# Performance work log

Measured on AMD Instinct MI355X. Metric: run time of the kernel, lower is better.

## Reference

```python
import jax, jax.numpy as jnp
import numpy as np

B, C, H, W = 8, 512, 32, 32
NH, DH = 8, 64          # num_heads, head_dim (C = NH*DH)
GROUPS, EPS = 32, 1e-5


def group_norm(x, gamma, beta):
    b, c, h, w = x.shape
    xg = x.reshape(b, GROUPS, c // GROUPS, h, w)
    mu = xg.mean(axis=(2, 3, 4), keepdims=True)
    var = xg.var(axis=(2, 3, 4), keepdims=True)
    xn = ((xg - mu) * jax.lax.rsqrt(var + EPS)).reshape(b, c, h, w)
    return xn * gamma[:, None, None] + beta[:, None, None]


def conv1x1(x, w, b):
    # x: [B,C,H,W], w: [O,C], b: [O]
    return jnp.einsum('bchw,oc->bohw', x, w) + b[:, None, None]


def setup_inputs() -> dict:
    key = jax.random.key(0)
    ks = jax.random.split(key, 5)
    return {
        'x': jax.random.normal(ks[0], (B, C, H, W), jnp.float32),
        'norm_gamma': jnp.ones((C,), jnp.float32),
        'norm_beta': jnp.zeros((C,), jnp.float32),
        'qkv_w': jax.random.normal(ks[1], (3 * C, C), jnp.float32) * (1.0 / np.sqrt(C)),
        'qkv_b': jax.random.normal(ks[2], (3 * C,), jnp.float32) * 0.02,
        'proj_w': jax.random.normal(ks[3], (C, C), jnp.float32) * (1.0 / np.sqrt(C)),
        'proj_b': jax.random.normal(ks[4], (C,), jnp.float32) * 0.02,
    }


def reference(x, norm_gamma, norm_beta, qkv_w, qkv_b, proj_w, proj_b):
    scale = DH ** -0.5
    h = group_norm(x, norm_gamma, norm_beta)
    qkv = conv1x1(h, qkv_w, qkv_b)                       # [B,3C,H,W]
    qkv = qkv.reshape(B, 3, NH, DH, H * W)
    qkv = jnp.transpose(qkv, (1, 0, 2, 4, 3))            # [3,B,NH,HW,DH]
    q, k, v = qkv[0], qkv[1], qkv[2]
    attn = jnp.einsum('bhid,bhjd->bhij', q, k) * scale   # [B,NH,HW,HW]
    attn = jax.nn.softmax(attn, axis=-1)
    h = jnp.einsum('bhij,bhjd->bhid', attn, v)           # [B,NH,HW,DH]
    # faithful to torch: direct row-major reshape [B,NH,HW,DH] -> [B,C,H,W]
    h = h.reshape(B, C, H, W)
    h = conv1x1(h, proj_w, proj_b)
    return x + h
```

## Files before the change

kernel.cpp:

```cpp
#include <hip/hip_runtime.h>


typedef float  f32x4  __attribute__((ext_vector_type(4)));
typedef float  f32x16 __attribute__((ext_vector_type(16)));
typedef __bf16 bf16x8 __attribute__((ext_vector_type(8)));
typedef __bf16 bf16x4 __attribute__((ext_vector_type(4)));
typedef __bf16 bf16x2 __attribute__((ext_vector_type(2)));

#define MFMA(a, b, c)   __builtin_amdgcn_mfma_f32_16x16x32_bf16(a, b, c, 0, 0, 0)
#define MFMA32(a, b, c) __builtin_amdgcn_mfma_f32_32x32x16_bf16(a, b, c, 0, 0, 0)

__device__ __forceinline__ void async16(const __bf16* g, __bf16* l) {
  __builtin_amdgcn_global_load_lds((const __attribute__((address_space(1))) void*)g,
                                   (__attribute__((address_space(3))) void*)l, 16, 0, 0);
}

__device__ __forceinline__ int chk(int n, int c) {
  return ((((n >> 6) * 16 + (c >> 5)) * 4 + ((c >> 3) & 3)) * 512) + (n & 63) * 8 + (c & 7);
}

__global__ __launch_bounds__(512) void prep_k(const float* __restrict__ x,
                                              const float* __restrict__ gamma,
                                              const float* __restrict__ beta,
                                              __bf16* __restrict__ Hout,
                                              const float* __restrict__ qw, __bf16* __restrict__ dq,
                                              const float* __restrict__ pw, __bf16* __restrict__ dp) {
  __shared__ __bf16 xs[16 * 1032];
  __shared__ float  red[16];
  __shared__ float  ga[16], be[16], stat[2];
  const int tid = threadIdx.x;

  if (blockIdx.x >= 256) {
    int i = ((blockIdx.x - 256) * 512 + tid) * 4;
    const float* src = (i < 786432) ? qw : pw;
    __bf16* dst = (i < 786432) ? dq : dp;
    int j = (i < 786432) ? i : (i - 786432);
    int m = j >> 9, k = j & 511;
    float4 v = *(const float4*)(src + j);
    bf16x4 o;
    o[0] = (__bf16)v.x; o[1] = (__bf16)v.y; o[2] = (__bf16)v.z; o[3] = (__bf16)v.w;
    *(bf16x4*)(dst + chk(m, k)) = o;
    return;
  }

  const int w = tid >> 6, l = tid & 63;
  const int bg = blockIdx.x, b = bg >> 5, g = bg & 31, c0 = g * 16;
  const float* xg = x + b * 524288 + c0 * 1024;

  float sum = 0.f, sq = 0.f;
#pragma unroll
  for (int p = 0; p < 8; p++) {
    int idx = p * 2048 + tid * 4;
    float4 v = *(const float4*)(xg + idx);
    int c = idx >> 10, s = idx & 1023;
    bf16x4 o;
    o[0] = (__bf16)v.x; o[1] = (__bf16)v.y; o[2] = (__bf16)v.z; o[3] = (__bf16)v.w;
    *(bf16x4*)(&xs[c * 1032 + s]) = o;
    sum += v.x + v.y + v.z + v.w;
    sq  += v.x * v.x + v.y * v.y + v.z * v.z + v.w * v.w;
  }
#pragma unroll
  for (int o = 32; o > 0; o >>= 1) { sum += __shfl_down(sum, o); sq += __shfl_down(sq, o); }
  if (l == 0) { red[w * 2] = sum; red[w * 2 + 1] = sq; }
  __syncthreads();
  if (tid == 0) {
    float S = 0.f, Q = 0.f;
#pragma unroll
    for (int i = 0; i < 8; i++) { S += red[i * 2]; Q += red[i * 2 + 1]; }
    float mean = S * (1.f / 16384.f);
    float var  = Q * (1.f / 16384.f) - mean * mean;
    stat[0] = mean; stat[1] = rsqrtf(var + 1e-5f);
  }
  if (tid < 16) { ga[tid] = gamma[c0 + tid]; be[tid] = beta[c0 + tid]; }
  __syncthreads();
  const float mean = stat[0], rstd = stat[1];
#pragma unroll
  for (int p = 0; p < 2; p++) {
    int s = p * 512 + tid;
    int n = b * 1024 + s;
    bf16x8 o0, o1;
#pragma unroll
    for (int c = 0; c < 8; c++) {
      float f = (float)xs[c * 1032 + s];
      o0[c] = (__bf16)((f - mean) * rstd * ga[c] + be[c]);
    }
#pragma unroll
    for (int c = 8; c < 16; c++) {
      float f = (float)xs[c * 1032 + s];
      o1[c - 8] = (__bf16)((f - mean) * rstd * ga[c] + be[c]);
    }
    *(bf16x8*)(Hout + chk(n, c0)) = o0;
    *(bf16x8*)(Hout + chk(n, c0 + 8)) = o1;
  }
}

__global__ __launch_bounds__(256) void gemm_qkv_k(const __bf16* __restrict__ W,
                                                  const float* __restrict__ bias,
                                                  const __bf16* __restrict__ H,
                                                  __bf16* __restrict__ qbuf,
                                                  __bf16* __restrict__ kbuf,
                                                  __bf16* __restrict__ vt) {
  __shared__ union {
    struct { __bf16 a[2][4096]; __bf16 b[2][4096]; } ab;
    __bf16 cs[128 * 136];
  } lds;
  const int tid = threadIdx.x;
  const int w = tid >> 6, l = tid & 63, quad = l >> 4, li = l & 15;
  const int wr = w >> 1, wc = w & 1;
  const int mblk = blockIdx.x >> 6, nblk = blockIdx.x & 63;
  const int m0 = mblk * 128, n0 = nblk * 128;

  f32x4 acc[4][4];
#pragma unroll
  for (int i = 0; i < 4; i++)
#pragma unroll
    for (int j = 0; j < 4; j++) acc[i][j] = f32x4{0.f, 0.f, 0.f, 0.f};

  const __bf16* Ag = W + (((m0 >> 6) * 16) * 4 + w) * 512 + l * 8;
  const __bf16* Bg = H + (((n0 >> 6) * 16) * 4 + w) * 512 + l * 8;
  const int halfA = 16 * 4 * 512;

  async16(Ag,         &lds.ab.a[0][w * 1024]);
  async16(Ag + halfA, &lds.ab.a[0][w * 1024 + 512]);
  async16(Bg,         &lds.ab.b[0][w * 1024]);
  async16(Bg + halfA, &lds.ab.b[0][w * 1024 + 512]);

#pragma unroll 1
  for (int kt = 0; kt < 16; kt++) {
    int cur = kt & 1, nxt = cur ^ 1;
    __syncthreads();
    if (kt < 15) {
      int ko = (kt + 1) * 2048;
      async16(Ag + ko,          &lds.ab.a[nxt][w * 1024]);
      async16(Ag + halfA + ko,  &lds.ab.a[nxt][w * 1024 + 512]);
      async16(Bg + ko,          &lds.ab.b[nxt][w * 1024]);
      async16(Bg + halfA + ko,  &lds.ab.b[nxt][w * 1024 + 512]);
    }
    bf16x8 af[4], bfr[4];
#pragma unroll
    for (int i = 0; i < 4; i++)
      af[i] = *(const bf16x8*)(&lds.ab.a[cur][quad * 1024 + (wr * 64 + i * 16 + li) * 8]);
#pragma unroll
    for (int i = 0; i < 4; i++)
      bfr[i] = *(const bf16x8*)(&lds.ab.b[cur][quad * 1024 + (wc * 64 + i * 16 + li) * 8]);
#pragma unroll
    for (int i = 0; i < 4; i++)
#pragma unroll
      for (int j = 0; j < 4; j++) acc[i][j] = MFMA(af[i], bfr[j], acc[i][j]);
  }

  const int t = m0 >> 9;
  const int cbase = m0 & 511;
  __syncthreads();
#pragma unroll
  for (int mi = 0; mi < 4; mi++) {
    int olocal = wr * 64 + mi * 16 + quad * 4;
    float bs[4];
#pragma unroll
    for (int r = 0; r < 4; r++) bs[r] = bias[m0 + olocal + r];
#pragma unroll
    for (int ni = 0; ni < 4; ni++) {
      int nlocal = wc * 64 + ni * 16 + li;
      bf16x4 pk;
#pragma unroll
      for (int r = 0; r < 4; r++) {
        float f = acc[mi][ni][r] + bs[r];
        if (t == 0) f *= 0.180336880f;
        pk[r] = (__bf16)f;
      }
      *(bf16x4*)(&lds.cs[nlocal * 136 + olocal]) = pk;
    }
  }
  __syncthreads();
  const int bb = n0 >> 10, s0 = n0 & 1023;
  if (t < 2) {
    __bf16* dst = (t == 0) ? qbuf : kbuf;
    const int nh0 = cbase >> 6;
#pragma unroll
    for (int p = 0; p < 8; p++) {
      int idx = p * 256 + tid;
      int oc = idx & 15, nloc = idx >> 4;
      uint4 val = *(const uint4*)(&lds.cs[nloc * 136 + oc * 8]);
      int bh = bb * 8 + nh0 + (oc >> 3);
      int s = s0 + nloc, d0 = (oc & 7) * 8;
      *(uint4*)(dst + (((bh * 16 + (s >> 6)) * 8 + (d0 >> 3)) * 64 + (s & 63)) * 8) = val;
    }
  } else {
#pragma unroll
    for (int p = 0; p < 8; p++) {
      int idx = p * 256 + tid;
      int o = idx & 127, ng = idx >> 7;
      int c = cbase + o, nh2 = c >> 6, d = c & 63;
      int bh = bb * 8 + nh2;
      int j0 = s0 + ng * 8;
      bf16x8 vv;
#pragma unroll
      for (int jj = 0; jj < 8; jj++) vv[jj] = lds.cs[(ng * 8 + jj) * 136 + o];
      *(bf16x8*)(vt + (((bh * 16 + (j0 >> 6)) * 8 + ((j0 >> 3) & 7)) * 64 + d) * 8) = vv;
    }
  }
}

__global__ __launch_bounds__(256) void attn_k(const __bf16* __restrict__ qb,
                                              const __bf16* __restrict__ kb,
                                              const __bf16* __restrict__ vt,
                                              __bf16* __restrict__ pin) {
  __shared__ __bf16 KC[2][4096];
  __shared__ __bf16 VC[2][4096];
  __shared__ __bf16 PO[8192];
  const int tid = threadIdx.x;
  const int w = tid >> 6, l = tid & 63, hi = l >> 5, i32 = l & 31;
  const int x = blockIdx.x;
  const int qt = (x >> 3) & 7;
  const int bh = (x & 7) | ((x >> 6) << 3);
  const int b = bh >> 3, nh = bh & 7;
  const __bf16* Qg = qb + bh * 65536;
  const __bf16* Kg = kb + bh * 65536;
  const __bf16* Vg = vt + bh * 65536;

#pragma unroll
  for (int p = 0; p < 2; p++) {
    int ch = w + 4 * p;
    async16(Kg + ch * 512 + l * 8, &KC[0][ch * 512 + l * 8]);
    async16(Vg + ch * 512 + l * 8, &VC[0][ch * 512 + l * 8]);
  }

  const int s = qt * 128 + w * 32 + i32;
  bf16x8 qf[4];
#pragma unroll
  for (int ks = 0; ks < 4; ks++)
    qf[ks] = *(const bf16x8*)(Qg + ((s >> 6) * 8 + ks * 2 + hi) * 512 + (s & 63) * 8);

  __syncthreads();

  const int swz = (i32 & 7) << 4;
  char* Pw = (char*)PO + w * 4096;
  float lsum = 0.f;
  f32x16 oacc[2];
#pragma unroll
  for (int r = 0; r < 16; r++) { oacc[0][r] = 0.f; oacc[1][r] = 0.f; }

#pragma unroll 1
  for (int kv = 0; kv < 16; kv++) {
    int cur = kv & 1, nxt = cur ^ 1;
    if (kv < 15) {
#pragma unroll
      for (int p = 0; p < 2; p++) {
        int ch = w + 4 * p;
        async16(Kg + (kv + 1) * 4096 + ch * 512 + l * 8, &KC[nxt][ch * 512 + l * 8]);
        async16(Vg + (kv + 1) * 4096 + ch * 512 + l * 8, &VC[nxt][ch * 512 + l * 8]);
      }
    }

    f32x16 st[2];
#pragma unroll
    for (int r = 0; r < 16; r++) { st[0][r] = 0.f; st[1][r] = 0.f; }
#pragma unroll
    for (int ks = 0; ks < 4; ks++) {
#pragma unroll
      for (int jt = 0; jt < 2; jt++) {
        bf16x8 kf = *(const bf16x8*)(&KC[cur][(ks * 2 + hi) * 512 + (jt * 32 + i32) * 8]);
        st[jt] = MFMA32(kf, qf[ks], st[jt]);
      }
    }

#pragma unroll
    for (int jt = 0; jt < 2; jt++) {
#pragma unroll
      for (int q2 = 0; q2 < 4; q2++) {
        float p0 = __builtin_amdgcn_exp2f(st[jt][q2 * 4 + 0]);
        float p1 = __builtin_amdgcn_exp2f(st[jt][q2 * 4 + 1]);
        float p2 = __builtin_amdgcn_exp2f(st[jt][q2 * 4 + 2]);
        float p3 = __builtin_amdgcn_exp2f(st[jt][q2 * 4 + 3]);
        lsum += (p0 + p1) + (p2 + p3);
        bf16x4 pk;
        pk[0] = (__bf16)p0; pk[1] = (__bf16)p1; pk[2] = (__bf16)p2; pk[3] = (__bf16)p3;
        *(bf16x4*)(Pw + ((i32 * 128 + jt * 64 + q2 * 16 + hi * 8) ^ swz)) = pk;
      }
    }

#pragma unroll
    for (int js = 0; js < 4; js++) {
      bf16x8 pf = *(const bf16x8*)(Pw + ((i32 * 128 + js * 32 + hi * 16) ^ swz));
#pragma unroll
      for (int dt = 0; dt < 2; dt++) {
        bf16x8 vf = *(const bf16x8*)(&VC[cur][(js * 2 + hi) * 512 + (dt * 32 + i32) * 8]);
        oacc[dt] = MFMA32(pf, vf, oacc[dt]);
      }
    }
    __syncthreads();
  }

  lsum += __shfl_xor(lsum, 32);
  const float inv = 1.f / lsum;

#pragma unroll
  for (int dt = 0; dt < 2; dt++) {
#pragma unroll
    for (int r = 0; r < 8; r++) {
      int ilo = (r & 3) + 8 * (r >> 2) + 4 * hi;
      float iblo = __shfl(inv, ilo);
      float ibhi = __shfl(inv, ilo + 16);
      bf16x2 ov;
      ov[0] = (__bf16)(oacc[dt][r]     * iblo);
      ov[1] = (__bf16)(oacc[dt][r + 8] * ibhi);
      *(bf16x2*)((char*)PO + (ilo * 64 + dt * 32 + i32) * 16 + w * 4) = ov;
    }
  }
  __syncthreads();
  __bf16* Pg = pin + (nh * 8 + qt) * 65536 + b * 8192;
#pragma unroll
  for (int p = 0; p < 4; p++) {
    int idx = p * 256 + tid;
    *(bf16x8*)(Pg + idx * 8) = *(const bf16x8*)((const char*)PO + idx * 16);
  }
}

__global__ __launch_bounds__(256) void gemm_proj_k(const __bf16* __restrict__ W,
                                                   const float* __restrict__ bias,
                                                   const __bf16* __restrict__ P,
                                                   const float* __restrict__ x,
                                                   float* __restrict__ out) {
  __shared__ __bf16 AL[2][2048];
  __shared__ __bf16 BL[2][4096];
  const int tid = threadIdx.x;
  const int w = tid >> 6, l = tid & 63, quad = l >> 4, li = l & 15;
  const int wr = w >> 1, wc = w & 1;
  const int mblk = blockIdx.x >> 6, nblk = blockIdx.x & 63;
  const int m0 = mblk * 64, n0 = nblk * 128;

  f32x4 acc[2][4];
#pragma unroll
  for (int i = 0; i < 2; i++)
#pragma unroll
    for (int j = 0; j < 4; j++) acc[i][j] = f32x4{0.f, 0.f, 0.f, 0.f};

  const __bf16* Ag = W + ((mblk * 16) * 4 + w) * 512 + l * 8;
  const __bf16* Bg = P + w * 65536 + (n0 + l) * 8;

  async16(Ag,       &AL[0][w * 512]);
  async16(Bg,       &BL[0][w * 1024]);
  async16(Bg + 512, &BL[0][w * 1024 + 512]);

#pragma unroll 1
  for (int kt = 0; kt < 16; kt++) {
    int cur = kt & 1, nxt = cur ^ 1;
    __syncthreads();
    if (kt < 15) {
      int koA = (kt + 1) * 2048;
      int koB = (kt + 1) * 262144;
      async16(Ag + koA,       &AL[nxt][w * 512]);
      async16(Bg + koB,       &BL[nxt][w * 1024]);
      async16(Bg + koB + 512, &BL[nxt][w * 1024 + 512]);
    }
    bf16x8 af[2], bfr[4];
#pragma unroll
    for (int i = 0; i < 2; i++)
      af[i] = *(const bf16x8*)(&AL[cur][quad * 512 + (wr * 32 + i * 16 + li) * 8]);
#pragma unroll
    for (int j = 0; j < 4; j++)
      bfr[j] = *(const bf16x8*)(&BL[cur][quad * 1024 + (wc * 64 + j * 16 + li) * 8]);
#pragma unroll
    for (int i = 0; i < 2; i++)
#pragma unroll
      for (int j = 0; j < 4; j++) acc[i][j] = MFMA(af[i], bfr[j], acc[i][j]);
  }

  const int bb = n0 >> 10;
#pragma unroll
  for (int mi = 0; mi < 2; mi++) {
    int o = m0 + wr * 32 + mi * 16 + quad * 4;
    float bs[4];
#pragma unroll
    for (int r = 0; r < 4; r++) bs[r] = bias[o + r];
#pragma unroll
    for (int ni = 0; ni < 4; ni++) {
      int n = n0 + wc * 64 + ni * 16 + li;
      int s = n & 1023;
#pragma unroll
      for (int r = 0; r < 4; r++) {
        int a = (bb * 512 + o + r) * 1024 + s;
        out[a] = acc[mi][ni][r] + bs[r] + x[a];
      }
    }
  }
}

extern "C" void kernel_launch(void* const* d_in, const int* in_sizes, int n_in,
                              void* d_out, int out_size, void* d_ws, size_t ws_size,
                              hipStream_t stream) {
  const float* x      = (const float*)d_in[0];
  const float* gamma  = (const float*)d_in[1];
  const float* beta   = (const float*)d_in[2];
  const float* qkv_w  = (const float*)d_in[3];
  const float* qkv_b  = (const float*)d_in[4];
  const float* proj_w = (const float*)d_in[5];
  const float* proj_b = (const float*)d_in[6];

  __bf16* ws   = (__bf16*)d_ws;
  __bf16* H    = ws;
  __bf16* qbuf = ws + 4194304;
  __bf16* kbuf = ws + 8388608;
  __bf16* vt   = ws + 12582912;
  __bf16* wq   = ws + 16777216;
  __bf16* wp   = ws + 17563648;

  prep_k<<<768, 512, 0, stream>>>(x, gamma, beta, H, qkv_w, wq, proj_w, wp);
  gemm_qkv_k<<<768, 256, 0, stream>>>(wq, qkv_b, H, qbuf, kbuf, vt);
  attn_k<<<512, 256, 0, stream>>>(qbuf, kbuf, vt, H);
  gemm_proj_k<<<512, 256, 0, stream>>>(wp, proj_b, H, x, (float*)d_out);
}
```

Measured before the change: 143.2 us.

## Fuse all four stages into one persistent kernel with grid barriers

Replaces the four separate launches (groupnorm/weight-convert, QKV GEMM, attention, projection GEMM) with a single 768-block megakernel. The stages are separated by atomic-counter grid barriers, and each stage reuses one shared LDS buffer. The goal is to remove the launch gaps and tail effects between kernels. It relies on all 768 blocks being co-resident (3 per CU under launch bounds), adds spin-barrier and memset overhead, and leaves blocks idle in the 512-block stages. The attention score loop is also reordered so each 32-column tile is computed and exponentiated before the next, which lowers register pressure.

```diff
diff --git a/kernel.cpp b/kernel.cpp
--- a/kernel.cpp
+++ b/kernel.cpp
@@ -19,368 +19,355 @@
   return ((((n >> 6) * 16 + (c >> 5)) * 4 + ((c >> 3) & 3)) * 512) + (n & 63) * 8 + (c & 7);
 }
 
-__global__ __launch_bounds__(512) void prep_k(const float* __restrict__ x,
-                                              const float* __restrict__ gamma,
-                                              const float* __restrict__ beta,
-                                              __bf16* __restrict__ Hout,
-                                              const float* __restrict__ qw, __bf16* __restrict__ dq,
-                                              const float* __restrict__ pw, __bf16* __restrict__ dp) {
-  __shared__ __bf16 xs[16 * 1032];
-  __shared__ float  red[16];
-  __shared__ float  ga[16], be[16], stat[2];
-  const int tid = threadIdx.x;
-
-  if (blockIdx.x >= 256) {
-    int i = ((blockIdx.x - 256) * 512 + tid) * 4;
-    const float* src = (i < 786432) ? qw : pw;
-    __bf16* dst = (i < 786432) ? dq : dp;
-    int j = (i < 786432) ? i : (i - 786432);
-    int m = j >> 9, k = j & 511;
-    float4 v = *(const float4*)(src + j);
-    bf16x4 o;
-    o[0] = (__bf16)v.x; o[1] = (__bf16)v.y; o[2] = (__bf16)v.z; o[3] = (__bf16)v.w;
-    *(bf16x4*)(dst + chk(m, k)) = o;
-    return;
-  }
-
-  const int w = tid >> 6, l = tid & 63;
-  const int bg = blockIdx.x, b = bg >> 5, g = bg & 31, c0 = g * 16;
-  const float* xg = x + b * 524288 + c0 * 1024;
-
-  float sum = 0.f, sq = 0.f;
-#pragma unroll
-  for (int p = 0; p < 8; p++) {
-    int idx = p * 2048 + tid * 4;
-    float4 v = *(const float4*)(xg + idx);
-    int c = idx >> 10, s = idx & 1023;
-    bf16x4 o;
-    o[0] = (__bf16)v.x; o[1] = (__bf16)v.y; o[2] = (__bf16)v.z; o[3] = (__bf16)v.w;
-    *(bf16x4*)(&xs[c * 1032 + s]) = o;
-    sum += v.x + v.y + v.z + v.w;
-    sq  += v.x * v.x + v.y * v.y + v.z * v.z + v.w * v.w;
-  }
-#pragma unroll
-  for (int o = 32; o > 0; o >>= 1) { sum += __shfl_down(sum, o); sq += __shfl_down(sq, o); }
-  if (l == 0) { red[w * 2] = sum; red[w * 2 + 1] = sq; }
+__device__ __forceinline__ void gbar(unsigned* c) {
   __syncthreads();
-  if (tid == 0) {
-    float S = 0.f, Q = 0.f;
-#pragma unroll
-    for (int i = 0; i < 8; i++) { S += red[i * 2]; Q += red[i * 2 + 1]; }
-    float mean = S * (1.f / 16384.f);
-    float var  = Q * (1.f / 16384.f) - mean * mean;
-    stat[0] = mean; stat[1] = rsqrtf(var + 1e-5f);
-  }
-  if (tid < 16) { ga[tid] = gamma[c0 + tid]; be[tid] = beta[c0 + tid]; }
-  __syncthreads();
-  const float mean = stat[0], rstd = stat[1];
-#pragma unroll
-  for (int p = 0; p < 2; p++) {
-    int s = p * 512 + tid;
-    int n = b * 1024 + s;
-    bf16x8 o0, o1;
-#pragma unroll
-    for (int c = 0; c < 8; c++) {
-      float f = (float)xs[c * 1032 + s];
-      o0[c] = (__bf16)((f - mean) * rstd * ga[c] + be[c]);
-    }
-#pragma unroll
-    for (int c = 8; c < 16; c++) {
-      float f = (float)xs[c * 1032 + s];
-      o1[c - 8] = (__bf16)((f - mean) * rstd * ga[c] + be[c]);
-    }
-    *(bf16x8*)(Hout + chk(n, c0)) = o0;
-    *(bf16x8*)(Hout + chk(n, c0 + 8)) = o1;
-  }
-}
-
-__global__ __launch_bounds__(256) void gemm_qkv_k(const __bf16* __restrict__ W,
-                                                  const float* __restrict__ bias,
-                                                  const __bf16* __restrict__ H,
-                                                  __bf16* __restrict__ qbuf,
-                                                  __bf16* __restrict__ kbuf,
-                                                  __bf16* __restrict__ vt) {
-  __shared__ union {
-    struct { __bf16 a[2][4096]; __bf16 b[2][4096]; } ab;
-    __bf16 cs[128 * 136];
-  } lds;
-  const int tid = threadIdx.x;
-  const int w = tid >> 6, l = tid & 63, quad = l >> 4, li = l & 15;
-  const int wr = w >> 1, wc = w & 1;
-  const int mblk = blockIdx.x >> 6, nblk = blockIdx.x & 63;
-  const int m0 = mblk * 128, n0 = nblk * 128;
-
-  f32x4 acc[4][4];
-#pragma unroll
-  for (int i = 0; i < 4; i++)
-#pragma unroll
-    for (int j = 0; j < 4; j++) acc[i][j] = f32x4{0.f, 0.f, 0.f, 0.f};
-
-  const __bf16* Ag = W + (((m0 >> 6) * 16) * 4 + w) * 512 + l * 8;
-  const __bf16* Bg = H + (((n0 >> 6) * 16) * 4 + w) * 512 + l * 8;
-  const int halfA = 16 * 4 * 512;
-
-  async16(Ag,         &lds.ab.a[0][w * 1024]);
-  async16(Ag + halfA, &lds.ab.a[0][w * 1024 + 512]);
-  async16(Bg,         &lds.ab.b[0][w * 1024]);
-  async16(Bg + halfA, &lds.ab.b[0][w * 1024 + 512]);
-
-#pragma unroll 1
-  for (int kt = 0; kt < 16; kt++) {
-    int cur = kt & 1, nxt = cur ^ 1;
-    __syncthreads();
-    if (kt < 15) {
-      int ko = (kt + 1) * 2048;
-      async16(Ag + ko,          &lds.ab.a[nxt][w * 1024]);
-      async16(Ag + halfA + ko,  &lds.ab.a[nxt][w * 1024 + 512]);
-      async16(Bg + ko,          &lds.ab.b[nxt][w * 1024]);
-      async16(Bg + halfA + ko,  &lds.ab.b[nxt][w * 1024 + 512]);
-    }
-    bf16x8 af[4], bfr[4];
-#pragma unroll
-    for (int i = 0; i < 4; i++)
-      af[i] = *(const bf16x8*)(&lds.ab.a[cur][quad * 1024 + (wr * 64 + i * 16 + li) * 8]);
-#pragma unroll
-    for (int i = 0; i < 4; i++)
-      bfr[i] = *(const bf16x8*)(&lds.ab.b[cur][quad * 1024 + (wc * 64 + i * 16 + li) * 8]);
-#pragma unroll
-    for (int i = 0; i < 4; i++)
-#pragma unroll
-      for (int j = 0; j < 4; j++) acc[i][j] = MFMA(af[i], bfr[j], acc[i][j]);
-  }
-
-  const int t = m0 >> 9;
-  const int cbase = m0 & 511;
-  __syncthreads();
-#pragma unroll
-  for (int mi = 0; mi < 4; mi++) {
-    int olocal = wr * 64 + mi * 16 + quad * 4;
-    float bs[4];
-#pragma unroll
-    for (int r = 0; r < 4; r++) bs[r] = bias[m0 + olocal + r];
-#pragma unroll
-    for (int ni = 0; ni < 4; ni++) {
-      int nlocal = wc * 64 + ni * 16 + li;
-      bf16x4 pk;
-#pragma unroll
-      for (int r = 0; r < 4; r++) {
-        float f = acc[mi][ni][r] + bs[r];
-        if (t == 0) f *= 0.180336880f;
-        pk[r] = (__bf16)f;
-      }
-      *(bf16x4*)(&lds.cs[nlocal * 136 + olocal]) = pk;
-    }
+  if (threadIdx.x == 0) {
+    __threadfence();
+    atomicAdd(c, 1u);
+    while (atomicAdd(c, 0u) < 768u) __builtin_amdgcn_s_sleep(8);
+    __threadfence();
   }
   __syncthreads();
-  const int bb = n0 >> 10, s0 = n0 & 1023;
-  if (t < 2) {
-    __bf16* dst = (t == 0) ? qbuf : kbuf;
-    const int nh0 = cbase >> 6;
-#pragma unroll
-    for (int p = 0; p < 8; p++) {
+}
+
+__global__ __launch_bounds__(256, 3) void mega_k(
+    const float* __restrict__ x, const float* __restrict__ gamma, const float* __restrict__ beta,
+    const float* __restrict__ qw, const float* __restrict__ qkv_b,
+    const float* __restrict__ pw, const float* __restrict__ proj_b,
+    __bf16* __restrict__ H, __bf16* __restrict__ qbuf, __bf16* __restrict__ kbuf,
+    __bf16* __restrict__ vt, __bf16* __restrict__ wq, __bf16* __restrict__ wp,
+    float* __restrict__ out, unsigned* __restrict__ bar) {
+  __shared__ __align__(16) char smem[49152];
+  const int tid = threadIdx.x, bid = blockIdx.x;
+
+  if (bid < 256) {
+    __bf16* xs  = (__bf16*)smem;
+    float* red  = (float*)(smem + 33024);
+    float* ga   = (float*)(smem + 33024 + 32);
+    float* be   = ga + 16;
+    float* stat = be + 16;
+    const int w = tid >> 6, l = tid & 63;
+    const int b = bid >> 5, g = bid & 31, c0 = g * 16;
+    const float* xg = x + b * 524288 + c0 * 1024;
+    float sum = 0.f, sq = 0.f;
+#pragma unroll
+    for (int c = 0; c < 16; c++) {
+      float4 v = *(const float4*)(xg + c * 1024 + tid * 4);
+      bf16x4 o;
+      o[0] = (__bf16)v.x; o[1] = (__bf16)v.y; o[2] = (__bf16)v.z; o[3] = (__bf16)v.w;
+      *(bf16x4*)(&xs[c * 1032 + tid * 4]) = o;
+      sum += v.x + v.y + v.z + v.w;
+      sq  += v.x * v.x + v.y * v.y + v.z * v.z + v.w * v.w;
+    }
+#pragma unroll
+    for (int o = 32; o > 0; o >>= 1) { sum += __shfl_down(sum, o); sq += __shfl_down(sq, o); }
+    if (l == 0) { red[w * 2] = sum; red[w * 2 + 1] = sq; }
+    __syncthreads();
+    if (tid == 0) {
+      float S = 0.f, Q = 0.f;
+#pragma unroll
+      for (int i = 0; i < 4; i++) { S += red[i * 2]; Q += red[i * 2 + 1]; }
+      float mean = S * (1.f / 16384.f);
+      float var  = Q * (1.f / 16384.f) - mean * mean;
+      stat[0] = mean; stat[1] = rsqrtf(var + 1e-5f);
+    }
+    if (tid < 16) { ga[tid] = gamma[c0 + tid]; be[tid] = beta[c0 + tid]; }
+    __syncthreads();
+    const float mean = stat[0], rstd = stat[1];
+#pragma unroll
+    for (int p = 0; p < 4; p++) {
+      int sx = p * 256 + tid;
+      int n = b * 1024 + sx;
+      bf16x8 o0, o1;
+#pragma unroll
+      for (int c = 0; c < 8; c++)
+        o0[c] = (__bf16)(((float)xs[c * 1032 + sx] - mean) * rstd * ga[c] + be[c]);
+#pragma unroll
+      for (int c = 8; c < 16; c++)
+        o1[c - 8] = (__bf16)(((float)xs[c * 1032 + sx] - mean) * rstd * ga[c] + be[c]);
+      *(bf16x8*)(H + chk(n, c0)) = o0;
+      *(bf16x8*)(H + chk(n, c0 + 8)) = o1;
+    }
+  } else {
+#pragma unroll
+    for (int sweep = 0; sweep < 2; sweep++) {
+      int i = ((bid - 256) * 256 + tid) * 4 + sweep * 524288;
+      const float* src = (i < 786432) ? qw : pw;
+      __bf16* dst = (i < 786432) ? wq : wp;
+      int j = (i < 786432) ? i : (i - 786432);
+      int m = j >> 9, k = j & 511;
+      float4 v = *(const float4*)(src + j);
+      bf16x4 o;
+      o[0] = (__bf16)v.x; o[1] = (__bf16)v.y; o[2] = (__bf16)v.z; o[3] = (__bf16)v.w;
+      *(bf16x4*)(dst + chk(m, k)) = o;
+    }
+  }
+  gbar(bar + 0);
+
+  {
+    __bf16 (*lA)[4096] = (__bf16(*)[4096])smem;
+    __bf16 (*lB)[4096] = (__bf16(*)[4096])(smem + 16384);
+    __bf16* cs         = (__bf16*)smem;
+    const int w = tid >> 6, l = tid & 63, quad = l >> 4, li = l & 15;
+    const int wr = w >> 1, wc = w & 1;
+    const int mblk = bid >> 6, nblk = bid & 63;
+    const int m0 = mblk * 128, n0 = nblk * 128;
+
+    f32x4 acc[4][4];
+#pragma unroll
+    for (int i = 0; i < 4; i++)
+#pragma unroll
+      for (int j = 0; j < 4; j++) acc[i][j] = f32x4{0.f, 0.f, 0.f, 0.f};
+
+    const __bf16* Ag = wq + (((m0 >> 6) * 16) * 4 + w) * 512 + l * 8;
+    const __bf16* Bg = H  + (((n0 >> 6) * 16) * 4 + w) * 512 + l * 8;
+    const int halfA = 16 * 4 * 512;
+
+    async16(Ag,         &lA[0][w * 1024]);
+    async16(Ag + halfA, &lA[0][w * 1024 + 512]);
+    async16(Bg,         &lB[0][w * 1024]);
+    async16(Bg + halfA, &lB[0][w * 1024 + 512]);
+
+#pragma unroll 1
+    for (int kt = 0; kt < 16; kt++) {
+      int cur = kt & 1, nxt = cur ^ 1;
+      __syncthreads();
+      if (kt < 15) {
+        int ko = (kt + 1) * 2048;
+        async16(Ag + ko,         &lA[nxt][w * 1024]);
+        async16(Ag + halfA + ko, &lA[nxt][w * 1024 + 512]);
+        async16(Bg + ko,         &lB[nxt][w * 1024]);
+        async16(Bg + halfA + ko, &lB[nxt][w * 1024 + 512]);
+      }
+      bf16x8 af[4], bfr[4];
+#pragma unroll
+      for (int i = 0; i < 4; i++)
+        af[i] = *(const bf16x8*)(&lA[cur][quad * 1024 + (wr * 64 + i * 16 + li) * 8]);
+#pragma unroll
+      for (int i = 0; i < 4; i++)
+        bfr[i] = *(const bf16x8*)(&lB[cur][quad * 1024 + (wc * 64 + i * 16 + li) * 8]);
+#pragma unroll
+      for (int i = 0; i < 4; i++)
+#pragma unroll
+        for (int j = 0; j < 4; j++) acc[i][j] = MFMA(af[i], bfr[j], acc[i][j]);
+    }
+
+    const int t = m0 >> 9;
+    const int cbase = m0 & 511;
+    __syncthreads();
+#pragma unroll
+    for (int mi = 0; mi < 4; mi++) {
+      int olocal = wr * 64 + mi * 16 + quad * 4;
+      float bs[4];
+#pragma unroll
+      for (int r = 0; r < 4; r++) bs[r] = qkv_b[m0 + olocal + r];
+#pragma unroll
+      for (int ni = 0; ni < 4; ni++) {
+        int nlocal = wc * 64 + ni * 16 + li;
+        bf16x4 pk;
+#pragma unroll
+        for (int r = 0; r < 4; r++) {
+          float f = acc[mi][ni][r] + bs[r];
+          if (t == 0) f *= 0.180336880f;
+          pk[r] = (__bf16)f;
+        }
+        *(bf16x4*)(&cs[nlocal * 136 + olocal]) = pk;
+      }
+    }
+    __syncthreads();
+    const int bb = n0 >> 10, s0 = n0 & 1023;
+    if (t < 2) {
+      __bf16* dst = (t == 0) ? qbuf : kbuf;
+      const int nh0 = cbase >> 6;
+#pragma unroll
+      for (int p = 0; p < 8; p++) {
+        int idx = p * 256 + tid;
+        int oc = idx & 15, nloc = idx >> 4;
+        uint4 val = *(const uint4*)(&cs[nloc * 136 + oc * 8]);
+        int bh = bb * 8 + nh0 + (oc >> 3);
+        int s = s0 + nloc, d0 = (oc & 7) * 8;
+        *(uint4*)(dst + (((bh * 16 + (s >> 6)) * 8 + (d0 >> 3)) * 64 + (s & 63)) * 8) = val;
+      }
+    } else {
+#pragma unroll
+      for (int p = 0; p < 8; p++) {
+        int idx = p * 256 + tid;
+        int o = idx & 127, ng = idx >> 7;
+        int c = cbase + o, nh2 = c >> 6, d = c & 63;
+        int bh = bb * 8 + nh2;
+        int j0 = s0 + ng * 8;
+        bf16x8 vv;
+#pragma unroll
+        for (int jj = 0; jj < 8; jj++) vv[jj] = cs[(ng * 8 + jj) * 136 + o];
+        *(bf16x8*)(vt + (((bh * 16 + (j0 >> 6)) * 8 + ((j0 >> 3) & 7)) * 64 + d) * 8) = vv;
+      }
+    }
+  }
+  gbar(bar + 1);
+
+  if (bid < 512) {
+    __bf16 (*KC)[4096] = (__bf16(*)[4096])smem;
+    __bf16 (*VC)[4096] = (__bf16(*)[4096])(smem + 16384);
+    __bf16* PO         = (__bf16*)(smem + 32768);
+    const int w = tid >> 6, l = tid & 63, hi = l >> 5, i32 = l & 31;
+    const int qt = (bid >> 3) & 7;
+    const int bh = (bid & 7) | ((bid >> 6) << 3);
+    const int b = bh >> 3, nh = bh & 7;
+    const __bf16* Qg = qbuf + bh * 65536;
+    const __bf16* Kg = kbuf + bh * 65536;
+    const __bf16* Vg = vt   + bh * 65536;
+
+#pragma unroll
+    for (int p = 0; p < 2; p++) {
+      int ch = w + 4 * p;
+      async16(Kg + ch * 512 + l * 8, &KC[0][ch * 512 + l * 8]);
+      async16(Vg + ch * 512 + l * 8, &VC[0][ch * 512 + l * 8]);
+    }
+    const int s = qt * 128 + w * 32 + i32;
+    bf16x8 qf[4];
+#pragma unroll
+    for (int ks = 0; ks < 4; ks++)
+      qf[ks] = *(const bf16x8*)(Qg + ((s >> 6) * 8 + ks * 2 + hi) * 512 + (s & 63) * 8);
+    __syncthreads();
+
+    const int swz = (i32 & 7) << 4;
+    char* Pw = (char*)PO + w * 4096;
+    float lsum = 0.f;
+    f32x16 oacc[2];
+#pragma unroll
+    for (int r = 0; r < 16; r++) { oacc[0][r] = 0.f; oacc[1][r] = 0.f; }
+
+#pragma unroll 1
+    for (int kv = 0; kv < 16; kv++) {
+      int cur = kv & 1, nxt = cur ^ 1;
+      if (kv < 15) {
+#pragma unroll
+        for (int p = 0; p < 2; p++) {
+          int ch = w + 4 * p;
+          async16(Kg + (kv + 1) * 4096 + ch * 512 + l * 8, &KC[nxt][ch * 512 + l * 8]);
+          async16(Vg + (kv + 1) * 4096 + ch * 512 + l * 8, &VC[nxt][ch * 512 + l * 8]);
+        }
+      }
+#pragma unroll
+      for (int jt = 0; jt < 2; jt++) {
+        f32x16 st;
+#pragma unroll
+        for (int r = 0; r < 16; r++) st[r] = 0.f;
+#pragma unroll
+        for (int ks = 0; ks < 4; ks++) {
+          bf16x8 kf = *(const bf16x8*)(&KC[cur][(ks * 2 + hi) * 512 + (jt * 32 + i32) * 8]);
+          st = MFMA32(kf, qf[ks], st);
+        }
+#pragma unroll
+        for (int q2 = 0; q2 < 4; q2++) {
+          float p0 = __builtin_amdgcn_exp2f(st[q2 * 4 + 0]);
+          float p1 = __builtin_amdgcn_exp2f(st[q2 * 4 + 1]);
+          float p2 = __builtin_amdgcn_exp2f(st[q2 * 4 + 2]);
+          float p3 = __builtin_amdgcn_exp2f(st[q2 * 4 + 3]);
+          lsum += (p0 + p1) + (p2 + p3);
+          bf16x4 pk;
+          pk[0] = (__bf16)p0; pk[1] = (__bf16)p1; pk[2] = (__bf16)p2; pk[3] = (__bf16)p3;
+          *(bf16x4*)(Pw + ((i32 * 128 + jt * 64 + q2 * 16 + hi * 8) ^ swz)) = pk;
+        }
+      }
+#pragma unroll
+      for (int js = 0; js < 4; js++) {
+        bf16x8 pf = *(const bf16x8*)(Pw + ((i32 * 128 + js * 32 + hi * 16) ^ swz));
+#pragma unroll
+        for (int dt = 0; dt < 2; dt++) {
+          bf16x8 vf = *(const bf16x8*)(&VC[cur][(js * 2 + hi) * 512 + (dt * 32 + i32) * 8]);
+          oacc[dt] = MFMA32(pf, vf, oacc[dt]);
+        }
+      }
+      __syncthreads();
+    }
+
+    lsum += __shfl_xor(lsum, 32);
+    const float inv = 1.f / lsum;
+#pragma unroll
+    for (int dt = 0; dt < 2; dt++) {
+#pragma unroll
+      for (int r = 0; r < 8; r++) {
+        int ilo = (r & 3) + 8 * (r >> 2) + 4 * hi;
+        float iblo = __shfl(inv, ilo);
+        float ibhi = __shfl(inv, ilo + 16);
+        bf16x2 ov;
+        ov[0] = (__bf16)(oacc[dt][r]     * iblo);
+        ov[1] = (__bf16)(oacc[dt][r + 8] * ibhi);
+        *(bf16x2*)((char*)PO + (ilo * 64 + dt * 32 + i32) * 16 + w * 4) = ov;
+      }
+    }
+    __syncthreads();
+    __bf16* Pg = H + (nh * 8 + qt) * 65536 + b * 8192;
+#pragma unroll
+    for (int p = 0; p < 4; p++) {
       int idx = p * 256 + tid;
-      int oc = idx & 15, nloc = idx >> 4;
-      uint4 val = *(const uint4*)(&lds.cs[nloc * 136 + oc * 8]);
-      int bh = bb * 8 + nh0 + (oc >> 3);
-      int s = s0 + nloc, d0 = (oc & 7) * 8;
-      *(uint4*)(dst + (((bh * 16 + (s >> 6)) * 8 + (d0 >> 3)) * 64 + (s & 63)) * 8) = val;
-    }
-  } else {
-#pragma unroll
-    for (int p = 0; p < 8; p++) {
-      int idx = p * 256 + tid;
-      int o = idx & 127, ng = idx >> 7;
-      int c = cbase + o, nh2 = c >> 6, d = c & 63;
-      int bh = bb * 8 + nh2;
-      int j0 = s0 + ng * 8;
-      bf16x8 vv;
-#pragma unroll
-      for (int jj = 0; jj < 8; jj++) vv[jj] = lds.cs[(ng * 8 + jj) * 136 + o];
-      *(bf16x8*)(vt + (((bh * 16 + (j0 >> 6)) * 8 + ((j0 >> 3) & 7)) * 64 + d) * 8) = vv;
+      *(bf16x8*)(Pg + idx * 8) = *(const bf16x8*)((const char*)PO + idx * 16);
     }
   }
-}
-
-__global__ __launch_bounds__(256) void attn_k(const __bf16* __restrict__ qb,
-                                              const __bf16* __restrict__ kb,
-                                              const __bf16* __restrict__ vt,
-                                              __bf16* __restrict__ pin) {
-  __shared__ __bf16 KC[2][4096];
-  __shared__ __bf16 VC[2][4096];
-  __shared__ __bf16 PO[8192];
-  const int tid = threadIdx.x;
-  const int w = tid >> 6, l = tid & 63, hi = l >> 5, i32 = l & 31;
-  const int x = blockIdx.x;
-  const int qt = (x >> 3) & 7;
-  const int bh = (x & 7) | ((x >> 6) << 3);
-  const int b = bh >> 3, nh = bh & 7;
-  const __bf16* Qg = qb + bh * 65536;
-  const __bf16* Kg = kb + bh * 65536;
-  const __bf16* Vg = vt + bh * 65536;
-
-#pragma unroll
-  for (int p = 0; p < 2; p++) {
-    int ch = w + 4 * p;
-    async16(Kg + ch * 512 + l * 8, &KC[0][ch * 512 + l * 8]);
-    async16(Vg + ch * 512 + l * 8, &VC[0][ch * 512 + l * 8]);
-  }
-
-  const int s = qt * 128 + w * 32 + i32;
-  bf16x8 qf[4];
-#pragma unroll
-  for (int ks = 0; ks < 4; ks++)
-    qf[ks] = *(const bf16x8*)(Qg + ((s >> 6) * 8 + ks * 2 + hi) * 512 + (s & 63) * 8);
-
-  __syncthreads();
-
-  const int swz = (i32 & 7) << 4;
-  char* Pw = (char*)PO + w * 4096;
-  float lsum = 0.f;
-  f32x16 oacc[2];
-#pragma unroll
-  for (int r = 0; r < 16; r++) { oacc[0][r] = 0.f; oacc[1][r] = 0.f; }
+  gbar(bar + 2);
+
+  if (bid < 512) {
+    __bf16 (*AL)[2048] = (__bf16(*)[2048])smem;
+    __bf16 (*BL)[4096] = (__bf16(*)[4096])(smem + 8192);
+    const int w = tid >> 6, l = tid & 63, quad = l >> 4, li = l & 15;
+    const int wr = w >> 1, wc = w & 1;
+    const int mblk = bid >> 6, nblk = bid & 63;
+    const int m0 = mblk * 64, n0 = nblk * 128;
+
+    f32x4 acc[2][4];
+#pragma unroll
+    for (int i = 0; i < 2; i++)
+#pragma unroll
+      for (int j = 0; j < 4; j++) acc[i][j] = f32x4{0.f, 0.f, 0.f, 0.f};
+
+    const __bf16* Ag = wp + ((mblk * 16) * 4 + w) * 512 + l * 8;
+    const __bf16* Bg = H  + w * 65536 + (n0 + l) * 8;
+
+    async16(Ag,       &AL[0][w * 512]);
+    async16(Bg,       &BL[0][w * 1024]);
+    async16(Bg + 512, &BL[0][w * 1024 + 512]);
 
 #pragma unroll 1
-  for (int kv = 0; kv < 16; kv++) {
-    int cur = kv & 1, nxt = cur ^ 1;
-    if (kv < 15) {
-#pragma unroll
-      for (int p = 0; p < 2; p++) {
-        int ch = w + 4 * p;
-        async16(Kg + (kv + 1) * 4096 + ch * 512 + l * 8, &KC[nxt][ch * 512 + l * 8]);
-        async16(Vg + (kv + 1) * 4096 + ch * 512 + l * 8, &VC[nxt][ch * 512 + l * 8]);
-      }
-    }
-
-    f32x16 st[2];
-#pragma unroll
-    for (int r = 0; r < 16; r++) { st[0][r] = 0.f; st[1][r] = 0.f; }
-#pragma unroll
-    for (int ks = 0; ks < 4; ks++) {
-#pragma unroll
-      for (int jt = 0; jt < 2; jt++) {
-        bf16x8 kf = *(const bf16x8*)(&KC[cur][(ks * 2 + hi) * 512 + (jt * 32 + i32) * 8]);
-        st[jt] = MFMA32(kf, qf[ks], st[jt]);
-      }
-    }
-
-#pragma unroll
-    for (int jt = 0; jt < 2; jt++) {
-#pragma unroll
-      for (int q2 = 0; q2 < 4; q2++) {
-        float p0 = __builtin_amdgcn_exp2f(st[jt][q2 * 4 + 0]);
-        float p1 = __builtin_amdgcn_exp2f(st[jt][q2 * 4 + 1]);
-        float p2 = __builtin_amdgcn_exp2f(st[jt][q2 * 4 + 2]);
-        float p3 = __builtin_amdgcn_exp2f(st[jt][q2 * 4 + 3]);
-        lsum += (p0 + p1) + (p2 + p3);
-        bf16x4 pk;
-        pk[0] = (__bf16)p0; pk[1] = (__bf16)p1; pk[2] = (__bf16)p2; pk[3] = (__bf16)p3;
-        *(bf16x4*)(Pw + ((i32 * 128 + jt * 64 + q2 * 16 + hi * 8) ^ swz)) = pk;
-      }
-    }
-
-#pragma unroll
-    for (int js = 0; js < 4; js++) {
-      bf16x8 pf = *(const bf16x8*)(Pw + ((i32 * 128 + js * 32 + hi * 16) ^ swz));
-#pragma unroll
-      for (int dt = 0; dt < 2; dt++) {
-        bf16x8 vf = *(const bf16x8*)(&VC[cur][(js * 2 + hi) * 512 + (dt * 32 + i32) * 8]);
-        oacc[dt] = MFMA32(pf, vf, oacc[dt]);
-      }
-    }
-    __syncthreads();
-  }
-
-  lsum += __shfl_xor(lsum, 32);
-  const float inv = 1.f / lsum;
-
-#pragma unroll
-  for (int dt = 0; dt < 2; dt++) {
-#pragma unroll
-    for (int r = 0; r < 8; r++) {
-      int ilo = (r & 3) + 8 * (r >> 2) + 4 * hi;
-      float iblo = __shfl(inv, ilo);
-      float ibhi = __shfl(inv, ilo + 16);
-      bf16x2 ov;
-      ov[0] = (__bf16)(oacc[dt][r]     * iblo);
-      ov[1] = (__bf16)(oacc[dt][r + 8] * ibhi);
-      *(bf16x2*)((char*)PO + (ilo * 64 + dt * 32 + i32) * 16 + w * 4) = ov;
-    }
-  }
-  __syncthreads();
-  __bf16* Pg = pin + (nh * 8 + qt) * 65536 + b * 8192;
-#pragma unroll
-  for (int p = 0; p < 4; p++) {
-    int idx = p * 256 + tid;
-    *(bf16x8*)(Pg + idx * 8) = *(const bf16x8*)((const char*)PO + idx * 16);
-  }
-}
-
-__global__ __launch_bounds__(256) void gemm_proj_k(const __bf16* __restrict__ W,
-                                                   const float* __restrict__ bias,
-                                                   const __bf16* __restrict__ P,
-                                                   const float* __restrict__ x,
-                                                   float* __restrict__ out) {
-  __shared__ __bf16 AL[2][2048];
-  __shared__ __bf16 BL[2][4096];
-  const int tid = threadIdx.x;
-  const int w = tid >> 6, l = tid & 63, quad = l >> 4, li = l & 15;
-  const int wr = w >> 1, wc = w & 1;
-  const int mblk = blockIdx.x >> 6, nblk = blockIdx.x & 63;
-  const int m0 = mblk * 64, n0 = nblk * 128;
-
-  f32x4 acc[2][4];
-#pragma unroll
-  for (int i = 0; i < 2; i++)
-#pragma unroll
-    for (int j = 0; j < 4; j++) acc[i][j] = f32x4{0.f, 0.f, 0.f, 0.f};
-
-  const __bf16* Ag = W + ((mblk * 16) * 4 + w) * 512 + l * 8;
-  const __bf16* Bg = P + w * 65536 + (n0 + l) * 8;
-
-  async16(Ag,       &AL[0][w * 512]);
-  async16(Bg,       &BL[0][w * 1024]);
-  async16(Bg + 512, &BL[0][w * 1024 + 512]);
-
-#pragma unroll 1
-  for (int kt = 0; kt < 16; kt++) {
-    int cur = kt & 1, nxt = cur ^ 1;
-    __syncthreads();
-    if (kt < 15) {
-      int koA = (kt + 1) * 2048;
-      int koB = (kt + 1) * 262144;
-      async16(Ag + koA,       &AL[nxt][w * 512]);
-      async16(Bg + koB,       &BL[nxt][w * 1024]);
-      async16(Bg + koB + 512, &BL[nxt][w * 1024 + 512]);
-    }
-    bf16x8 af[2], bfr[4];
-#pragma unroll
-    for (int i = 0; i < 2; i++)
-      af[i] = *(const bf16x8*)(&AL[cur][quad * 512 + (wr * 32 + i * 16 + li) * 8]);
-#pragma unroll
-    for (int j = 0; j < 4; j++)
-      bfr[j] = *(const bf16x8*)(&BL[cur][quad * 1024 + (wc * 64 + j * 16 + li) * 8]);
-#pragma unroll
-    for (int i = 0; i < 2; i++)
-#pragma unroll
-      for (int j = 0; j < 4; j++) acc[i][j] = MFMA(af[i], bfr[j], acc[i][j]);
-  }
-
-  const int bb = n0 >> 10;
-#pragma unroll
-  for (int mi = 0; mi < 2; mi++) {
-    int o = m0 + wr * 32 + mi * 16 + quad * 4;
-    float bs[4];
-#pragma unroll
-    for (int r = 0; r < 4; r++) bs[r] = bias[o + r];
-#pragma unroll
-    for (int ni = 0; ni < 4; ni++) {
-      int n = n0 + wc * 64 + ni * 16 + li;
-      int s = n & 1023;
-#pragma unroll
-      for (int r = 0; r < 4; r++) {
-        int a = (bb * 512 + o + r) * 1024 + s;
-        out[a] = acc[mi][ni][r] + bs[r] + x[a];
+    for (int kt = 0; kt < 16; kt++) {
+      int cur = kt & 1, nxt = cur ^ 1;
+      __syncthreads();
+      if (kt < 15) {
+        int koA = (kt + 1) * 2048;
+        int koB = (kt + 1) * 262144;
+        async16(Ag + koA,       &AL[nxt][w * 512]);
+        async16(Bg + koB,       &BL[nxt][w * 1024]);
+        async16(Bg + koB + 512, &BL[nxt][w * 1024 + 512]);
+      }
+      bf16x8 af[2], bfr[4];
+#pragma unroll
+      for (int i = 0; i < 2; i++)
+        af[i] = *(const bf16x8*)(&AL[cur][quad * 512 + (wr * 32 + i * 16 + li) * 8]);
+#pragma unroll
+      for (int j = 0; j < 4; j++)
+        bfr[j] = *(const bf16x8*)(&BL[cur][quad * 1024 + (wc * 64 + j * 16 + li) * 8]);
+#pragma unroll
+      for (int i = 0; i < 2; i++)
+#pragma unroll
+        for (int j = 0; j < 4; j++) acc[i][j] = MFMA(af[i], bfr[j], acc[i][j]);
+    }
+
+    const int bb = n0 >> 10;
+#pragma unroll
+    for (int mi = 0; mi < 2; mi++) {
+      int o = m0 + wr * 32 + mi * 16 + quad * 4;
+      float bs[4];
+#pragma unroll
+      for (int r = 0; r < 4; r++) bs[r] = proj_b[o + r];
+#pragma unroll
+      for (int ni = 0; ni < 4; ni++) {
+        int n = n0 + wc * 64 + ni * 16 + li;
+        int sx = n & 1023;
+#pragma unroll
+        for (int r = 0; r < 4; r++) {
+          int a = (bb * 512 + o + r) * 1024 + sx;
+          out[a] = acc[mi][ni][r] + bs[r] + x[a];
+        }
       }
     }
   }
@@ -405,8 +392,10 @@
   __bf16* wq   = ws + 16777216;
   __bf16* wp   = ws + 17563648;
 
-  prep_k<<<768, 512, 0, stream>>>(x, gamma, beta, H, qkv_w, wq, proj_w, wp);
-  gemm_qkv_k<<<768, 256, 0, stream>>>(wq, qkv_b, H, qbuf, kbuf, vt);
-  attn_k<<<512, 256, 0, stream>>>(qbuf, kbuf, vt, H);
-  gemm_proj_k<<<512, 256, 0, stream>>>(wp, proj_b, H, x, (float*)d_out);
+  size_t boff = (ws_size - 256) & ~(size_t)63;
+  unsigned* bar = (unsigned*)((char*)d_ws + boff);
+  hipMemsetAsync(bar, 0, 64, stream);
+
+  mega_k<<<768, 256, 0, stream>>>(x, gamma, beta, qkv_w, qkv_b, proj_w, proj_b,
+                                  H, qbuf, kbuf, vt, wq, wp, (float*)d_out, bar);
 }
```

Result: slower. 385.5 us (+169.2%).

## Read K/V tiles directly from global memory in attention, drop LDS double buffer

Applied to the files above, without the earlier changes.

The attention kernel no longer stages K and V tiles in LDS through async global-to-LDS loads with double buffering. Each wave now loads its K and V fragments straight from global memory (cache-backed) and splits the score computation per 32-key subtile, interleaved with the PV MFMAs. This removes the per-iteration block barrier and the LDS traffic and footprint, which may allow more blocks per CU. The cost is that each of the 4 waves re-reads the same K/V data from L1/L2 with no explicit prefetch, so global load latency may be exposed inside the loop.

```diff
diff --git a/kernel.cpp b/kernel.cpp
--- a/kernel.cpp
+++ b/kernel.cpp
@@ -205,8 +205,6 @@
                                               const __bf16* __restrict__ kb,
                                               const __bf16* __restrict__ vt,
                                               __bf16* __restrict__ pin) {
-  __shared__ __bf16 KC[2][4096];
-  __shared__ __bf16 VC[2][4096];
   __shared__ __bf16 PO[8192];
   const int tid = threadIdx.x;
   const int w = tid >> 6, l = tid & 63, hi = l >> 5, i32 = l & 31;
@@ -218,20 +216,11 @@
   const __bf16* Kg = kb + bh * 65536;
   const __bf16* Vg = vt + bh * 65536;
 
-#pragma unroll
-  for (int p = 0; p < 2; p++) {
-    int ch = w + 4 * p;
-    async16(Kg + ch * 512 + l * 8, &KC[0][ch * 512 + l * 8]);
-    async16(Vg + ch * 512 + l * 8, &VC[0][ch * 512 + l * 8]);
-  }
-
   const int s = qt * 128 + w * 32 + i32;
   bf16x8 qf[4];
 #pragma unroll
   for (int ks = 0; ks < 4; ks++)
     qf[ks] = *(const bf16x8*)(Qg + ((s >> 6) * 8 + ks * 2 + hi) * 512 + (s & 63) * 8);
-
-  __syncthreads();
 
   const int swz = (i32 & 7) << 4;
   char* Pw = (char*)PO + w * 4096;
@@ -242,57 +231,45 @@
 
 #pragma unroll 1
   for (int kv = 0; kv < 16; kv++) {
-    int cur = kv & 1, nxt = cur ^ 1;
-    if (kv < 15) {
-#pragma unroll
-      for (int p = 0; p < 2; p++) {
-        int ch = w + 4 * p;
-        async16(Kg + (kv + 1) * 4096 + ch * 512 + l * 8, &KC[nxt][ch * 512 + l * 8]);
-        async16(Vg + (kv + 1) * 4096 + ch * 512 + l * 8, &VC[nxt][ch * 512 + l * 8]);
-      }
-    }
-
-    f32x16 st[2];
-#pragma unroll
-    for (int r = 0; r < 16; r++) { st[0][r] = 0.f; st[1][r] = 0.f; }
-#pragma unroll
-    for (int ks = 0; ks < 4; ks++) {
-#pragma unroll
-      for (int jt = 0; jt < 2; jt++) {
-        bf16x8 kf = *(const bf16x8*)(&KC[cur][(ks * 2 + hi) * 512 + (jt * 32 + i32) * 8]);
-        st[jt] = MFMA32(kf, qf[ks], st[jt]);
-      }
-    }
-
+    const __bf16* Kt = Kg + kv * 4096;
+    const __bf16* Vt = Vg + kv * 4096;
 #pragma unroll
     for (int jt = 0; jt < 2; jt++) {
+      f32x16 st;
+#pragma unroll
+      for (int r = 0; r < 16; r++) st[r] = 0.f;
+#pragma unroll
+      for (int ks = 0; ks < 4; ks++) {
+        bf16x8 kf = *(const bf16x8*)(Kt + (ks * 2 + hi) * 512 + (jt * 32 + i32) * 8);
+        st = MFMA32(kf, qf[ks], st);
+      }
 #pragma unroll
       for (int q2 = 0; q2 < 4; q2++) {
-        float p0 = __builtin_amdgcn_exp2f(st[jt][q2 * 4 + 0]);
-        float p1 = __builtin_amdgcn_exp2f(st[jt][q2 * 4 + 1]);
-        float p2 = __builtin_amdgcn_exp2f(st[jt][q2 * 4 + 2]);
-        float p3 = __builtin_amdgcn_exp2f(st[jt][q2 * 4 + 3]);
+        float p0 = __builtin_amdgcn_exp2f(st[q2 * 4 + 0]);
+        float p1 = __builtin_amdgcn_exp2f(st[q2 * 4 + 1]);
+        float p2 = __builtin_amdgcn_exp2f(st[q2 * 4 + 2]);
+        float p3 = __builtin_amdgcn_exp2f(st[q2 * 4 + 3]);
         lsum += (p0 + p1) + (p2 + p3);
         bf16x4 pk;
         pk[0] = (__bf16)p0; pk[1] = (__bf16)p1; pk[2] = (__bf16)p2; pk[3] = (__bf16)p3;
         *(bf16x4*)(Pw + ((i32 * 128 + jt * 64 + q2 * 16 + hi * 8) ^ swz)) = pk;
       }
-    }
-
-#pragma unroll
-    for (int js = 0; js < 4; js++) {
-      bf16x8 pf = *(const bf16x8*)(Pw + ((i32 * 128 + js * 32 + hi * 16) ^ swz));
-#pragma unroll
-      for (int dt = 0; dt < 2; dt++) {
-        bf16x8 vf = *(const bf16x8*)(&VC[cur][(js * 2 + hi) * 512 + (dt * 32 + i32) * 8]);
-        oacc[dt] = MFMA32(pf, vf, oacc[dt]);
-      }
-    }
-    __syncthreads();
+#pragma unroll
+      for (int h = 0; h < 2; h++) {
+        int js = jt * 2 + h;
+        bf16x8 pf = *(const bf16x8*)(Pw + ((i32 * 128 + js * 32 + hi * 16) ^ swz));
+#pragma unroll
+        for (int dt = 0; dt < 2; dt++) {
+          bf16x8 vf = *(const bf16x8*)(Vt + (js * 2 + hi) * 512 + (dt * 32 + i32) * 8);
+          oacc[dt] = MFMA32(pf, vf, oacc[dt]);
+        }
+      }
+    }
   }
 
   lsum += __shfl_xor(lsum, 32);
   const float inv = 1.f / lsum;
+  __syncthreads();
 
 #pragma unroll
   for (int dt = 0; dt < 2; dt++) {
```

Measured after the change: 170.7 us. +19.2%, slower.

## Keep softmax probabilities in registers via permlane32 swap instead of LDS round-trip

Applied to the files above, without the earlier changes.

In the attention kernel, the exponentiated scores are no longer written to a swizzled LDS buffer and read back as the MFMA A operand. They are packed to bf16 pairs and rearranged across wave halves with v_permlane32_swap, then fed straight into the PV MFMA. The score computation is also restructured per 32-column tile, and the epilogue reuses the K buffer as its staging area. Together these drop a 16KB LDS array and its store/load traffic, which may raise occupancy. The risk is correctness, since it depends on the permlane swap producing exactly the operand layout the MFMA expects.

```diff
diff --git a/kernel.cpp b/kernel.cpp
--- a/kernel.cpp
+++ b/kernel.cpp
@@ -6,6 +6,7 @@
 typedef __bf16 bf16x8 __attribute__((ext_vector_type(8)));
 typedef __bf16 bf16x4 __attribute__((ext_vector_type(4)));
 typedef __bf16 bf16x2 __attribute__((ext_vector_type(2)));
+typedef unsigned u32x4 __attribute__((ext_vector_type(4)));
 
 #define MFMA(a, b, c)   __builtin_amdgcn_mfma_f32_16x16x32_bf16(a, b, c, 0, 0, 0)
 #define MFMA32(a, b, c) __builtin_amdgcn_mfma_f32_32x32x16_bf16(a, b, c, 0, 0, 0)
@@ -17,6 +18,11 @@
 
 __device__ __forceinline__ int chk(int n, int c) {
   return ((((n >> 6) * 16 + (c >> 5)) * 4 + ((c >> 3) & 3)) * 512) + (n & 63) * 8 + (c & 7);
+}
+
+__device__ __forceinline__ unsigned pk2(float x, float y) {
+  bf16x2 t; t[0] = (__bf16)x; t[1] = (__bf16)y;
+  return __builtin_bit_cast(unsigned, t);
 }
 
 __global__ __launch_bounds__(512) void prep_k(const float* __restrict__ x,
@@ -207,7 +213,6 @@
                                               __bf16* __restrict__ pin) {
   __shared__ __bf16 KC[2][4096];
   __shared__ __bf16 VC[2][4096];
-  __shared__ __bf16 PO[8192];
   const int tid = threadIdx.x;
   const int w = tid >> 6, l = tid & 63, hi = l >> 5, i32 = l & 31;
   const int x = blockIdx.x;
@@ -224,17 +229,13 @@
     async16(Kg + ch * 512 + l * 8, &KC[0][ch * 512 + l * 8]);
     async16(Vg + ch * 512 + l * 8, &VC[0][ch * 512 + l * 8]);
   }
-
   const int s = qt * 128 + w * 32 + i32;
   bf16x8 qf[4];
 #pragma unroll
   for (int ks = 0; ks < 4; ks++)
     qf[ks] = *(const bf16x8*)(Qg + ((s >> 6) * 8 + ks * 2 + hi) * 512 + (s & 63) * 8);
-
-  __syncthreads();
-
-  const int swz = (i32 & 7) << 4;
-  char* Pw = (char*)PO + w * 4096;
+  __syncthreads();
+
   float lsum = 0.f;
   f32x16 oacc[2];
 #pragma unroll
@@ -252,40 +253,37 @@
       }
     }
 
-    f32x16 st[2];
-#pragma unroll
-    for (int r = 0; r < 16; r++) { st[0][r] = 0.f; st[1][r] = 0.f; }
-#pragma unroll
-    for (int ks = 0; ks < 4; ks++) {
-#pragma unroll
-      for (int jt = 0; jt < 2; jt++) {
+#pragma unroll
+    for (int jt = 0; jt < 2; jt++) {
+      f32x16 st;
+#pragma unroll
+      for (int r = 0; r < 16; r++) st[r] = 0.f;
+#pragma unroll
+      for (int ks = 0; ks < 4; ks++) {
         bf16x8 kf = *(const bf16x8*)(&KC[cur][(ks * 2 + hi) * 512 + (jt * 32 + i32) * 8]);
-        st[jt] = MFMA32(kf, qf[ks], st[jt]);
+        st = MFMA32(kf, qf[ks], st);
       }
-    }
-
-#pragma unroll
-    for (int jt = 0; jt < 2; jt++) {
-#pragma unroll
-      for (int q2 = 0; q2 < 4; q2++) {
-        float p0 = __builtin_amdgcn_exp2f(st[jt][q2 * 4 + 0]);
-        float p1 = __builtin_amdgcn_exp2f(st[jt][q2 * 4 + 1]);
-        float p2 = __builtin_amdgcn_exp2f(st[jt][q2 * 4 + 2]);
-        float p3 = __builtin_amdgcn_exp2f(st[jt][q2 * 4 + 3]);
-        lsum += (p0 + p1) + (p2 + p3);
-        bf16x4 pk;
-        pk[0] = (__bf16)p0; pk[1] = (__bf16)p1; pk[2] = (__bf16)p2; pk[3] = (__bf16)p3;
-        *(bf16x4*)(Pw + ((i32 * 128 + jt * 64 + q2 * 16 + hi * 8) ^ swz)) = pk;
-      }
-    }
-
-#pragma unroll
-    for (int js = 0; js < 4; js++) {
-      bf16x8 pf = *(const bf16x8*)(Pw + ((i32 * 128 + js * 32 + hi * 16) ^ swz));
-#pragma unroll
-      for (int dt = 0; dt < 2; dt++) {
-        bf16x8 vf = *(const bf16x8*)(&VC[cur][(js * 2 + hi) * 512 + (dt * 32 + i32) * 8]);
-        oacc[dt] = MFMA32(pf, vf, oacc[dt]);
+      float pr[16];
+#pragma unroll
+      for (int r = 0; r < 16; r++) pr[r] = __builtin_amdgcn_exp2f(st[r]);
+#pragma unroll
+      for (int r = 0; r < 16; r += 4) lsum += (pr[r] + pr[r + 1]) + (pr[r + 2] + pr[r + 3]);
+#pragma unroll
+      for (int h = 0; h < 2; h++) {
+        unsigned u0 = pk2(pr[8 * h + 0], pr[8 * h + 1]);
+        unsigned u1 = pk2(pr[8 * h + 2], pr[8 * h + 3]);
+        unsigned v0 = pk2(pr[8 * h + 4], pr[8 * h + 5]);
+        unsigned v1 = pk2(pr[8 * h + 6], pr[8 * h + 7]);
+        asm volatile("v_permlane32_swap_b32 %0, %1" : "+v"(u0), "+v"(v0));
+        asm volatile("v_permlane32_swap_b32 %0, %1" : "+v"(u1), "+v"(v1));
+        u32x4 dv; dv[0] = u0; dv[1] = u1; dv[2] = v0; dv[3] = v1;
+        bf16x8 pf = __builtin_bit_cast(bf16x8, dv);
+        int js = jt * 2 + h;
+#pragma unroll
+        for (int dt = 0; dt < 2; dt++) {
+          bf16x8 vf = *(const bf16x8*)(&VC[cur][(js * 2 + hi) * 512 + (dt * 32 + i32) * 8]);
+          oacc[dt] = MFMA32(pf, vf, oacc[dt]);
+        }
       }
     }
     __syncthreads();
@@ -294,6 +292,7 @@
   lsum += __shfl_xor(lsum, 32);
   const float inv = 1.f / lsum;
 
+  char* PO = (char*)KC;
 #pragma unroll
   for (int dt = 0; dt < 2; dt++) {
 #pragma unroll
@@ -304,7 +303,7 @@
       bf16x2 ov;
       ov[0] = (__bf16)(oacc[dt][r]     * iblo);
       ov[1] = (__bf16)(oacc[dt][r + 8] * ibhi);
-      *(bf16x2*)((char*)PO + (ilo * 64 + dt * 32 + i32) * 16 + w * 4) = ov;
+      *(bf16x2*)(PO + (ilo * 64 + dt * 32 + i32) * 16 + w * 4) = ov;
     }
   }
   __syncthreads();
```

Measured after the change: 139.7 us, median of 4. 1.02x faster.
